# Kernel optimization log

Measured on AMD Instinct MI355X. Metric: run time of the kernel, lower is better.

## Reference

```python
import math
import jax, jax.numpy as jnp
import numpy as np

CAP_FACTOR_EVAL = 2.0   # eval mode, drop_tks=True path
MIN_CAPACITY = 4
S, E = 8192, 64


def _get_capacity(s, e):
    c = math.floor(CAP_FACTOR_EVAL * s / e)
    c += c % 2  # make even
    return max(c, MIN_CAPACITY)


def setup_inputs() -> dict:
    key = jax.random.key(0)
    return {"inputs": jax.random.normal(key, (S, E), dtype=jnp.float32)}


def reference(inputs):
    s, e = inputs.shape
    capacity = _get_capacity(s, e)  # static, from shapes only
    # autocast_softmax: softmax in fp32 over experts
    logits = jax.nn.softmax(inputs.astype(jnp.float32), axis=-1)      # [s, e]
    top1_idx = jnp.argmax(inputs, axis=-1)                             # [s]
    mask = jax.nn.one_hot(top1_idx, e, dtype=jnp.int32)                # [s, e]
    # moe_cumsum: exclusive cumsum over tokens per expert
    ranks = jnp.cumsum(mask, axis=0) - 1                               # [s, e]
    # 'first' select policy: keep only tokens whose rank fits capacity
    mask = mask * (ranks < capacity).astype(jnp.int32)                 # [s, e]
    rank1 = jnp.sum(mask * ranks, axis=-1)                             # [s] rank within chosen expert
    ranks_oh = jax.nn.one_hot(rank1, capacity, dtype=logits.dtype)     # [s, c]
    weight = mask.astype(logits.dtype) * logits                        # [s, e]
    combine_weights = weight[:, :, None] * ranks_oh[:, None, :]        # [s, e, c]
    sec_mask = combine_weights.astype(bool)
    return combine_weights, sec_mask
```

## Files before the change

### kernel.cpp

```cpp
#include <hip/hip_runtime.h>
#include <math.h>

#define NTOK 8192
#define NEXP 64
#define CAP  256
#define SEC  (NTOK * NEXP * CAP)

typedef float v4f __attribute__((ext_vector_type(4)));

__global__ __launch_bounds__(256) void k_top1(const float* __restrict__ in,
                                              int* __restrict__ top1,
                                              float* __restrict__ val) {
    int wave = threadIdx.x >> 6;
    int lane = threadIdx.x & 63;
    int s = blockIdx.x * 4 + wave;
    float x = in[s * NEXP + lane];

    float bv = x;
    int   bi = lane;
#pragma unroll
    for (int off = 32; off > 0; off >>= 1) {
        float ov = __shfl_xor(bv, off);
        int   oi = __shfl_xor(bi, off);
        if (ov > bv || (ov == bv && oi < bi)) { bv = ov; bi = oi; }
    }
    float ex = expf(x - bv);
#pragma unroll
    for (int off = 32; off > 0; off >>= 1) ex += __shfl_xor(ex, off);

    if (lane == 0) {
        top1[s] = bi;
        val[s]  = 1.0f / ex;
    }
}

__global__ __launch_bounds__(1024) void k_rank(const int* __restrict__ top1,
                                               int* __restrict__ rank) {
    __shared__ int localrank[NTOK];
    __shared__ int hist[16][64];
    __shared__ int chunkoff[16][64];

    int tid  = threadIdx.x;
    int w    = tid >> 6;
    int lane = tid & 63;
    int base = w * 512;

    int counter = 0;
    for (int j0 = 0; j0 < 512; j0 += 64) {
        int myidx  = top1[base + j0 + lane];
        int myrank = 0;
        for (int j = 0; j < 64; ++j) {
            int t = __shfl(myidx, j);
            int r = __shfl(counter, t);
            if (j == lane) myrank = r;
            counter += (lane == t) ? 1 : 0;
        }
        localrank[base + j0 + lane] = myrank;
    }
    hist[w][lane] = counter;
    __syncthreads();

    if (tid < 64) {
        int off = 0;
        for (int w2 = 0; w2 < 16; ++w2) {
            chunkoff[w2][tid] = off;
            off += hist[w2][tid];
        }
    }
    __syncthreads();

    for (int s = tid; s < NTOK; s += 1024) {
        int t = top1[s];
        rank[s] = localrank[s] + chunkoff[s >> 9][t];
    }
}

__global__ __launch_bounds__(256) void k_fill(const int* __restrict__ top1,
                                              const int* __restrict__ rank,
                                              const float* __restrict__ val,
                                              v4f* __restrict__ outc,
                                              v4f* __restrict__ outm) {
    int gid = blockIdx.x * 256 + threadIdx.x;
    int s = gid >> 12;
    int q4 = (gid & 4095) << 2;

    int   t = top1[s];
    int   r = rank[s];
    float v = val[s];
    bool keep = (r < CAP);
    int p = t * CAP + r;

    v4f c, m;
    c.x = (keep && p == q4 + 0) ? v : 0.0f;
    c.y = (keep && p == q4 + 1) ? v : 0.0f;
    c.z = (keep && p == q4 + 2) ? v : 0.0f;
    c.w = (keep && p == q4 + 3) ? v : 0.0f;
    m.x = (c.x != 0.0f) ? 1.0f : 0.0f;
    m.y = (c.y != 0.0f) ? 1.0f : 0.0f;
    m.z = (c.z != 0.0f) ? 1.0f : 0.0f;
    m.w = (c.w != 0.0f) ? 1.0f : 0.0f;

    __builtin_nontemporal_store(c, &outc[gid]);
    __builtin_nontemporal_store(m, &outm[gid]);
}

extern "C" void kernel_launch(void* const* d_in, const int* in_sizes, int n_in,
                              void* d_out, int out_size, void* d_ws, size_t ws_size,
                              hipStream_t stream) {
    const float* in = (const float*)d_in[0];

    int*   top1 = (int*)d_ws;
    float* val  = (float*)((char*)d_ws + NTOK * 4);
    int*   rank = (int*)((char*)d_ws + NTOK * 8);

    float* outc = (float*)d_out;
    float* outm = outc + (size_t)SEC;

    hipLaunchKernelGGL(k_top1, dim3(NTOK / 4), dim3(256), 0, stream, in, top1, val);
    hipLaunchKernelGGL(k_rank, dim3(1), dim3(1024), 0, stream, top1, rank);
    hipLaunchKernelGGL(k_fill, dim3(SEC / 4 / 256), dim3(256), 0, stream,
                       top1, rank, val, (v4f*)outc, (v4f*)outm);
}
```

Baseline: 1.067 ms.

## Use ballot-based match ranking and packed row info; widen fill stores

```diff
diff --git a/kernel.cpp b/kernel.cpp
--- a/kernel.cpp
+++ b/kernel.cpp
@@ -35,7 +35,8 @@
 }
 
 __global__ __launch_bounds__(1024) void k_rank(const int* __restrict__ top1,
-                                               int* __restrict__ rank) {
+                                               const float* __restrict__ val,
+                                               int2* __restrict__ rowinfo) {
     __shared__ int localrank[NTOK];
     __shared__ int hist[16][64];
     __shared__ int chunkoff[16][64];
@@ -45,19 +46,30 @@
     int lane = tid & 63;
     int base = w * 512;
 
-    int counter = 0;
+    int cnt = 0;
     for (int j0 = 0; j0 < 512; j0 += 64) {
-        int myidx  = top1[base + j0 + lane];
-        int myrank = 0;
-        for (int j = 0; j < 64; ++j) {
-            int t = __shfl(myidx, j);
-            int r = __shfl(counter, t);
-            if (j == lane) myrank = r;
-            counter += (lane == t) ? 1 : 0;
-        }
-        localrank[base + j0 + lane] = myrank;
+        int e = top1[base + j0 + lane];
+        unsigned long long b0 = __ballot((e & 1)  != 0);
+        unsigned long long b1 = __ballot((e & 2)  != 0);
+        unsigned long long b2 = __ballot((e & 4)  != 0);
+        unsigned long long b3 = __ballot((e & 8)  != 0);
+        unsigned long long b4 = __ballot((e & 16) != 0);
+        unsigned long long b5 = __ballot((e & 32) != 0);
+        unsigned long long my =
+            ((e & 1)  ? b0 : ~b0) & ((e & 2)  ? b1 : ~b1) &
+            ((e & 4)  ? b2 : ~b2) & ((e & 8)  ? b3 : ~b3) &
+            ((e & 16) ? b4 : ~b4) & ((e & 32) ? b5 : ~b5);
+        unsigned long long mb =
+            ((lane & 1)  ? b0 : ~b0) & ((lane & 2)  ? b1 : ~b1) &
+            ((lane & 4)  ? b2 : ~b2) & ((lane & 8)  ? b3 : ~b3) &
+            ((lane & 16) ? b4 : ~b4) & ((lane & 32) ? b5 : ~b5);
+
+        int lr  = __popcll(my & ((1ULL << lane) - 1ULL));
+        int off = __shfl(cnt, e);
+        localrank[base + j0 + lane] = off + lr;
+        cnt += __popcll(mb);
     }
-    hist[w][lane] = counter;
+    hist[w][lane] = cnt;
     __syncthreads();
 
     if (tid < 64) {
@@ -71,37 +83,37 @@
 
     for (int s = tid; s < NTOK; s += 1024) {
         int t = top1[s];
-        rank[s] = localrank[s] + chunkoff[s >> 9][t];
+        int r = localrank[s] + chunkoff[s >> 9][t];
+        int pos = (r < CAP) ? (t * CAP + r) : -1;
+        rowinfo[s] = make_int2(pos, __float_as_int(val[s]));
     }
 }
 
-__global__ __launch_bounds__(256) void k_fill(const int* __restrict__ top1,
-                                              const int* __restrict__ rank,
-                                              const float* __restrict__ val,
+__global__ __launch_bounds__(256) void k_fill(const int2* __restrict__ rowinfo,
                                               v4f* __restrict__ outc,
                                               v4f* __restrict__ outm) {
-    int gid = blockIdx.x * 256 + threadIdx.x;
+    int gid = (blockIdx.x * 256 + threadIdx.x) << 1;
     int s = gid >> 12;
-    int q4 = (gid & 4095) << 2;
+    int q = (gid & 4095) << 2;
 
-    int   t = top1[s];
-    int   r = rank[s];
-    float v = val[s];
-    bool keep = (r < CAP);
-    int p = t * CAP + r;
+    int2 ri = rowinfo[s];
+    float v = __int_as_float(ri.y);
+    int d = ri.x - q;
 
-    v4f c, m;
-    c.x = (keep && p == q4 + 0) ? v : 0.0f;
-    c.y = (keep && p == q4 + 1) ? v : 0.0f;
-    c.z = (keep && p == q4 + 2) ? v : 0.0f;
-    c.w = (keep && p == q4 + 3) ? v : 0.0f;
-    m.x = (c.x != 0.0f) ? 1.0f : 0.0f;
-    m.y = (c.y != 0.0f) ? 1.0f : 0.0f;
-    m.z = (c.z != 0.0f) ? 1.0f : 0.0f;
-    m.w = (c.w != 0.0f) ? 1.0f : 0.0f;
+    v4f c0, c1, m0, m1;
+    c0.x = (d == 0) ? v : 0.0f;  m0.x = (d == 0) ? 1.0f : 0.0f;
+    c0.y = (d == 1) ? v : 0.0f;  m0.y = (d == 1) ? 1.0f : 0.0f;
+    c0.z = (d == 2) ? v : 0.0f;  m0.z = (d == 2) ? 1.0f : 0.0f;
+    c0.w = (d == 3) ? v : 0.0f;  m0.w = (d == 3) ? 1.0f : 0.0f;
+    c1.x = (d == 4) ? v : 0.0f;  m1.x = (d == 4) ? 1.0f : 0.0f;
+    c1.y = (d == 5) ? v : 0.0f;  m1.y = (d == 5) ? 1.0f : 0.0f;
+    c1.z = (d == 6) ? v : 0.0f;  m1.z = (d == 6) ? 1.0f : 0.0f;
+    c1.w = (d == 7) ? v : 0.0f;  m1.w = (d == 7) ? 1.0f : 0.0f;
 
-    __builtin_nontemporal_store(c, &outc[gid]);
-    __builtin_nontemporal_store(m, &outm[gid]);
+    __builtin_nontemporal_store(c0, &outc[gid]);
+    __builtin_nontemporal_store(c1, &outc[gid + 1]);
+    __builtin_nontemporal_store(m0, &outm[gid]);
+    __builtin_nontemporal_store(m1, &outm[gid + 1]);
 }
 
 extern "C" void kernel_launch(void* const* d_in, const int* in_sizes, int n_in,
@@ -109,15 +121,15 @@
                               hipStream_t stream) {
     const float* in = (const float*)d_in[0];
 
-    int*   top1 = (int*)d_ws;
-    float* val  = (float*)((char*)d_ws + NTOK * 4);
-    int*   rank = (int*)((char*)d_ws + NTOK * 8);
+    int*   top1    = (int*)d_ws;
+    float* val     = (float*)((char*)d_ws + NTOK * 4);
+    int2*  rowinfo = (int2*)((char*)d_ws + NTOK * 8);
 
     float* outc = (float*)d_out;
     float* outm = outc + (size_t)SEC;
 
     hipLaunchKernelGGL(k_top1, dim3(NTOK / 4), dim3(256), 0, stream, in, top1, val);
-    hipLaunchKernelGGL(k_rank, dim3(1), dim3(1024), 0, stream, top1, rank);
-    hipLaunchKernelGGL(k_fill, dim3(SEC / 4 / 256), dim3(256), 0, stream,
-                       top1, rank, val, (v4f*)outc, (v4f*)outm);
+    hipLaunchKernelGGL(k_rank, dim3(1), dim3(1024), 0, stream, top1, val, rowinfo);
+    hipLaunchKernelGGL(k_fill, dim3(SEC / 4 / 2 / 256), dim3(256), 0, stream,
+                       rowinfo, (v4f*)outc, (v4f*)outm);
 }
```

Result: slower. 1.314 ms (+23.1%).
